# Kernel tuning notes

Measured on AMD Instinct MI355X. Metric: run time of the kernel, lower is better.

## Reference

```python
import jax, jax.numpy as jnp
import numpy as np

CHEB_K = 3


def cheb_gcn(x, node_emb, w_pool, b_pool):
    # x: [B, N, C], node_emb: [N, D], w_pool: [D, K, C, O], b_pool: [D, O]
    n = node_emb.shape[0]
    A = jax.nn.softmax(jax.nn.relu(node_emb @ node_emb.T), axis=1)  # [N, N]
    supports = [jnp.eye(n, dtype=x.dtype), A]
    for _ in range(2, CHEB_K):
        supports.append(2.0 * A @ supports[-1] - supports[-2])
    S = jnp.stack(supports, axis=0)  # [K, N, N]
    weights = jnp.einsum('nd,dkio->nkio', node_emb, w_pool)  # [N, K, C, O]
    bias = node_emb @ b_pool  # [N, O]
    x_g = jnp.einsum('knm,bmc->bnkc', S, x)  # [B, N, K, C]
    return jnp.einsum('bnki,nkio->bno', x_g, weights) + bias


def setup_inputs() -> dict:
    key = jax.random.key(0)
    ks = jax.random.split(key, 7)
    B, N, DIN, DOUT, E = 64, 1024, 64, 64, 16
    C = DIN + DOUT
    return {
        'x': jax.random.normal(ks[0], (B, N, DIN), jnp.float32),
        'state': jax.random.normal(ks[1], (B, N, DOUT), jnp.float32),
        'node_embeddings': jax.random.normal(ks[2], (N, E), jnp.float32),
        'W_gate': jax.random.normal(ks[3], (E, CHEB_K, C, 2 * DOUT), jnp.float32) * 0.1,
        'b_gate': jax.random.normal(ks[4], (E, 2 * DOUT), jnp.float32) * 0.1,
        'W_update': jax.random.normal(ks[5], (E, CHEB_K, C, DOUT), jnp.float32) * 0.1,
        'b_update': jax.random.normal(ks[6], (E, DOUT), jnp.float32) * 0.1,
    }


def reference(x, state, node_embeddings, W_gate, b_gate, W_update, b_update):
    hidden = state.shape[-1]
    inp = jnp.concatenate([x, state], axis=-1)  # [B, N, DIN+DOUT]
    z_r = jax.nn.sigmoid(cheb_gcn(inp, node_embeddings, W_gate, b_gate))
    z, r = z_r[..., :hidden], z_r[..., hidden:]
    cand = jnp.concatenate([x, r * state], axis=-1)
    h_hat = jnp.tanh(cheb_gcn(cand, node_embeddings, W_update, b_update))
    return z * state + (1.0 - z) * h_hat
```

## Files before the change

### kernel.cpp

```cpp
#include <hip/hip_runtime.h>
#include <hip/hip_bf16.h>
#include <math.h>

#define B_ 64
#define N_ 1024
#define E_ 16

typedef unsigned short ushort_t;
typedef __attribute__((ext_vector_type(8))) short bf16x8;
typedef __attribute__((ext_vector_type(4))) float f32x4;

__device__ __forceinline__ float sigmoidf_(float x) {
  return 1.0f / (1.0f + __expf(-x));
}
__device__ __forceinline__ ushort_t f2bf(float f) {
  unsigned int u = __float_as_uint(f);
  u = (u + 0x7fffu + ((u >> 16) & 1u)) >> 16;
  return (ushort_t)u;
}
__device__ __forceinline__ float bf2f(ushort_t h) { return __uint_as_float((unsigned)h << 16); }
__device__ __forceinline__ void gload16(const void* g, void* l) {
  __builtin_amdgcn_global_load_lds(
      (const __attribute__((address_space(1))) unsigned int*)g,
      (__attribute__((address_space(3))) unsigned int*)l, 16, 0, 0);
}

__global__ __launch_bounds__(256) void compute_A_kernel(const float* __restrict__ emb,
                                                        ushort_t* __restrict__ Ah,
                                                        ushort_t* __restrict__ Al) {
  __shared__ float embn[E_];
  __shared__ float red[256];
  const int n = blockIdx.x;
  const int t = threadIdx.x;
  if (t < E_) embn[t] = emb[n * E_ + t];
  __syncthreads();
  float s[4];
#pragma unroll
  for (int j = 0; j < 4; ++j) {
    const int m = j * 256 + t;
    const float* em = emb + m * E_;
    float acc = 0.f;
#pragma unroll
    for (int d = 0; d < E_; ++d) acc = fmaf(embn[d], em[d], acc);
    s[j] = fmaxf(acc, 0.f);
  }
  float mx = fmaxf(fmaxf(s[0], s[1]), fmaxf(s[2], s[3]));
  red[t] = mx;
  __syncthreads();
  for (int off = 128; off > 0; off >>= 1) {
    if (t < off) red[t] = fmaxf(red[t], red[t + off]);
    __syncthreads();
  }
  mx = red[0];
  __syncthreads();
  float e[4], lsum = 0.f;
#pragma unroll
  for (int j = 0; j < 4; ++j) { e[j] = __expf(s[j] - mx); lsum += e[j]; }
  red[t] = lsum;
  __syncthreads();
  for (int off = 128; off > 0; off >>= 1) {
    if (t < off) red[t] += red[t + off];
    __syncthreads();
  }
  const float inv = 1.0f / red[0];
#pragma unroll
  for (int j = 0; j < 4; ++j) {
    const float v = e[j] * inv;
    ushort_t h = f2bf(v);
    Ah[n * N_ + j * 256 + t] = h;
    Al[n * N_ + j * 256 + t] = f2bf(v - bf2f(h));
  }
}

__global__ __launch_bounds__(256) void build_T0t_kernel(const float* __restrict__ xA,
                                                        const float* __restrict__ xB,
                                                        ushort_t* __restrict__ Th,
                                                        ushort_t* __restrict__ Tl) {
  __shared__ float tile[128][129];
  const int t = threadIdx.x;
  const int b = blockIdx.y;
  const int n0 = blockIdx.x << 7;
  const int c4 = (t & 31) << 2, nl = t >> 5;
#pragma unroll
  for (int p = 0; p < 16; ++p) {
    const int n = nl + (p << 3);
    const float4 v = (c4 < 64)
        ? *(const float4*)&xA[((size_t)b << 16) + ((size_t)(n0 + n) << 6) + c4]
        : *(const float4*)&xB[((size_t)b << 16) + ((size_t)(n0 + n) << 6) + c4 - 64];
    tile[c4 + 0][n] = v.x; tile[c4 + 1][n] = v.y;
    tile[c4 + 2][n] = v.z; tile[c4 + 3][n] = v.w;
  }
  __syncthreads();
  const int c = t >> 1, nc = (t & 1) << 6;
  const size_t obase = ((size_t)(b << 7) + c) * 1024 + n0 + nc;
#pragma unroll
  for (int u = 0; u < 64; u += 4) {
    ushort4 h, l;
    float v0 = tile[c][nc + u + 0], v1 = tile[c][nc + u + 1];
    float v2 = tile[c][nc + u + 2], v3 = tile[c][nc + u + 3];
    h.x = f2bf(v0); l.x = f2bf(v0 - bf2f(h.x));
    h.y = f2bf(v1); l.y = f2bf(v1 - bf2f(h.y));
    h.z = f2bf(v2); l.z = f2bf(v2 - bf2f(h.z));
    h.w = f2bf(v3); l.w = f2bf(v3 - bf2f(h.w));
    *(ushort4*)&Th[obase + u] = h;
    *(ushort4*)&Tl[obase + u] = l;
  }
}

__global__ __launch_bounds__(256) void build_T0s_kernel(const float* __restrict__ rs,
                                                        ushort_t* __restrict__ Th,
                                                        ushort_t* __restrict__ Tl) {
  __shared__ float tile[64][129];
  const int t = threadIdx.x;
  const int b = blockIdx.y;
  const int n0 = blockIdx.x << 7;
  const int c4 = (t & 15) << 2, nl = t >> 4;
#pragma unroll
  for (int p = 0; p < 8; ++p) {
    const int n = nl + (p << 4);
    const float4 v = *(const float4*)&rs[((size_t)b << 16) + ((size_t)(n0 + n) << 6) + c4];
    tile[c4 + 0][n] = v.x; tile[c4 + 1][n] = v.y;
    tile[c4 + 2][n] = v.z; tile[c4 + 3][n] = v.w;
  }
  __syncthreads();
  const int c = t >> 2, nc = (t & 3) << 5;
  const size_t obase = ((size_t)(b << 6) + c) * 1024 + n0 + nc;
#pragma unroll
  for (int u = 0; u < 32; u += 4) {
    ushort4 h, l;
    float v0 = tile[c][nc + u + 0], v1 = tile[c][nc + u + 1];
    float v2 = tile[c][nc + u + 2], v3 = tile[c][nc + u + 3];
    h.x = f2bf(v0); l.x = f2bf(v0 - bf2f(h.x));
    h.y = f2bf(v1); l.y = f2bf(v1 - bf2f(h.y));
    h.z = f2bf(v2); l.z = f2bf(v2 - bf2f(h.z));
    h.w = f2bf(v3); l.w = f2bf(v3 - bf2f(h.w));
    *(ushort4*)&Th[obase + u] = h;
    *(ushort4*)&Tl[obase + u] = l;
  }
}

template <int PHASE, int SPAN>
__global__ __launch_bounds__(256, 2) void mfma_gemm_kernel(
    const ushort_t* __restrict__ Ah, const ushort_t* __restrict__ Al,
    const ushort_t* __restrict__ Bh, const ushort_t* __restrict__ Bl,
    ushort_t* __restrict__ Yth, ushort_t* __restrict__ Ytl,
    ushort_t* __restrict__ XpH, ushort_t* __restrict__ XpL) {
  __shared__ ushort_t smem[4 * 128 * 64];
  ushort_t* Ah_s = smem;
  ushort_t* Al_s = smem + 8192;
  ushort_t* Bh_s = smem + 16384;
  ushort_t* Bl_s = smem + 24576;
  const int t = threadIdx.x;
  const int wave = t >> 6, lane = t & 63;
  const int n0 = blockIdx.y << 7;
  const int bcol = blockIdx.x;
  const int j0 = bcol << 7;
  const int wr = wave >> 1, wc = wave & 1;
  const int fr = lane & 15, fk = lane >> 4;

  f32x4 acc[4][4];
#pragma unroll
  for (int i = 0; i < 4; ++i)
#pragma unroll
    for (int j = 0; j < 4; ++j) acc[i][j] = (f32x4){0.f, 0.f, 0.f, 0.f};

  const int rsub = lane >> 3;
  const int cp = lane & 7;
  const int selem = (((cp << 4) ^ (rsub << 4)) >> 1);

  for (int k0 = 0; k0 < 1024; k0 += 64) {
    __syncthreads();
#pragma unroll
    for (int i = 0; i < 4; ++i) {
      const int q = (wave << 2) + i;
      const int row = (q << 3) + rsub;
      const int lo = (q << 9) + lane * 8;
      const size_t ga = (size_t)(n0 + row) * 1024 + k0 + selem;
      const size_t gb = (size_t)(j0 + row) * 1024 + k0 + selem;
      gload16(Ah + ga, Ah_s + lo);
      gload16(Al + ga, Al_s + lo);
      gload16(Bh + gb, Bh_s + lo);
      gload16(Bl + gb, Bl_s + lo);
    }
    __syncthreads();
#pragma unroll
    for (int ks = 0; ks < 2; ++ks) {
      bf16x8 ah[4], al[4], bh[4], bl[4];
#pragma unroll
      for (int mi = 0; mi < 4; ++mi) {
        const int r = (wr << 6) + (mi << 4) + fr;
        const int kb = ((ks << 6) + (fk << 4)) ^ ((r & 7) << 4);
        ah[mi] = *(const bf16x8*)((const char*)Ah_s + r * 128 + kb);
        al[mi] = *(const bf16x8*)((const char*)Al_s + r * 128 + kb);
      }
#pragma unroll
      for (int nj = 0; nj < 4; ++nj) {
        const int r = (wc << 6) + (nj << 4) + fr;
        const int kb = ((ks << 6) + (fk << 4)) ^ ((r & 7) << 4);
        bh[nj] = *(const bf16x8*)((const char*)Bh_s + r * 128 + kb);
        bl[nj] = *(const bf16x8*)((const char*)Bl_s + r * 128 + kb);
      }
#pragma unroll
      for (int mi = 0; mi < 4; ++mi)
#pragma unroll
        for (int nj = 0; nj < 4; ++nj) {
          acc[mi][nj] = __builtin_amdgcn_mfma_f32_16x16x32_bf16(ah[mi], bh[nj], acc[mi][nj], 0, 0, 0);
          acc[mi][nj] = __builtin_amdgcn_mfma_f32_16x16x32_bf16(ah[mi], bl[nj], acc[mi][nj], 0, 0, 0);
          acc[mi][nj] = __builtin_amdgcn_mfma_f32_16x16x32_bf16(al[mi], bh[nj], acc[mi][nj], 0, 0, 0);
        }
    }
  }

  __syncthreads();
  ushort_t* hiT = smem;
  ushort_t* loT = smem + 16384;
#pragma unroll
  for (int mi = 0; mi < 4; ++mi) {
    const int nl = (wr << 6) + (mi << 4) + (fk << 2);
#pragma unroll
    for (int nj = 0; nj < 4; ++nj) {
      const int jl = (wc << 6) + (nj << 4) + fr;
      const f32x4 vv = acc[mi][nj];
      ushort_t h[4], l[4];
#pragma unroll
      for (int r = 0; r < 4; ++r) {
        const float v = (PHASE == 1) ? vv[r] : 2.0f * vv[r];
        h[r] = f2bf(v);
        l[r] = f2bf(v - bf2f(h[r]));
      }
      if (PHASE == 1) {
        *(ushort4*)&Yth[(size_t)(j0 + jl) * 1024 + n0 + nl] = make_ushort4(h[0], h[1], h[2], h[3]);
        *(ushort4*)&Ytl[(size_t)(j0 + jl) * 1024 + n0 + nl] = make_ushort4(l[0], l[1], l[2], l[3]);
      }
#pragma unroll
      for (int r = 0; r < 4; ++r) {
        hiT[(nl + r) * 128 + jl] = h[r];
        loT[(nl + r) * 128 + jl] = l[r];
      }
    }
  }
  __syncthreads();
#pragma unroll
  for (int rr = 0; rr < 8; ++rr) {
    const int id = rr * 256 + t;
    const int nl = id >> 4, ch = id & 15;
    size_t dstE;
    if (SPAN == 128) {
      dstE = ((size_t)(n0 + nl) * 64 + bcol) * 256 + ch * 8;
    } else {
      const int bb = bcol * 2 + (ch >> 3);
      dstE = ((size_t)(n0 + nl) * 64 + bb) * 256 + 64 + (ch & 7) * 8;
    }
    *(uint4*)&XpH[dstE] = *(const uint4*)((const char*)hiT + nl * 256 + ch * 16);
    *(uint4*)&XpL[dstE] = *(const uint4*)((const char*)loT + nl * 256 + ch * 16);
  }
}

template <int OW>
__global__ __launch_bounds__(256) void wpt_kernel(const float* __restrict__ Wp,
                                                  float* __restrict__ WpT) {
  const int idx = blockIdx.x * 256 + threadIdx.x;
  const int ki = idx % 384;
  const int k = ki >> 7, i = ki & 127;
  const int o = idx / 384;
  float v[16];
#pragma unroll
  for (int d = 0; d < 16; ++d) v[d] = Wp[((size_t)d * 384 + ki) * OW + o];
  if (k == 0) {
#pragma unroll
    for (int d = 0; d < 16; ++d) v[d] -= Wp[((size_t)d * 384 + 256 + i) * OW + o];
  }
  float* dst = WpT + (size_t)idx * 16;
#pragma unroll
  for (int q = 0; q < 4; ++q) *(float4*)&dst[q * 4] = *(const float4*)&v[q * 4];
}

__global__ __launch_bounds__(384) void wcombine5_kernel(const float* __restrict__ emb,
                                                        const float* __restrict__ WpT,
                                                        ushort_t* __restrict__ WtH,
                                                        ushort_t* __restrict__ WtL) {
  __shared__ float embs[256 * 16];
  __shared__ ushort_t sH[8 * 384];
  __shared__ ushort_t sL[8 * 384];
  const int t = threadIdx.x;
  const int o = blockIdx.y;
  const int n0 = blockIdx.x << 8;
  for (int i = t; i < 1024; i += 384)
    *(float4*)&embs[i * 4] = *(const float4*)&emb[(size_t)n0 * 16 + i * 4];
  float wreg[16];
  {
    const float* src = WpT + (size_t)o * 6144 + t * 16;
#pragma unroll
    for (int q = 0; q < 4; ++q) *(float4*)&wreg[q * 4] = *(const float4*)&src[q * 4];
  }
  __syncthreads();
  for (int g = 0; g < 32; ++g) {
#pragma unroll
    for (int nl = 0; nl < 8; ++nl) {
      const float* e = &embs[(g * 8 + nl) * 16];
      float a = 0.f;
#pragma unroll
      for (int d = 0; d < 16; ++d) a = fmaf(e[d], wreg[d], a);
      const ushort_t h = f2bf(a);
      sH[nl * 384 + t] = h;
      sL[nl * 384 + t] = f2bf(a - bf2f(h));
    }
    __syncthreads();
    const size_t ob = ((size_t)o * 1024 + n0 + g * 8) * 384 + t * 8;
    *(uint4*)&WtH[ob] = *(const uint4*)&sH[t * 8];
    *(uint4*)&WtL[ob] = *(const uint4*)&sL[t * 8];
    __syncthreads();
  }
}

template <int MODE>
__global__ __launch_bounds__(256, 2) void pernode_mfma_kernel(
    const float* __restrict__ xA, const float* __restrict__ xB,
    const ushort_t* __restrict__ XpH, const ushort_t* __restrict__ XpL,
    const ushort_t* __restrict__ WtH, const ushort_t* __restrict__ WtL,
    const float* __restrict__ emb, const float* __restrict__ bsrc, int bstride,
    const float* __restrict__ state, const float* __restrict__ zb,
    float* __restrict__ dst) {
  __shared__ ushort_t xh_s[64 * 128];
  __shared__ ushort_t xl_s[64 * 128];
  __shared__ ushort_t wh_s[64 * 128];
  __shared__ ushort_t wl_s[64 * 128];
  __shared__ float embn[E_];
  __shared__ float bias[64];
  const int n = blockIdx.x;
  const int t = threadIdx.x;
  if (t < E_) embn[t] = emb[n * E_ + t];
  __syncthreads();
  if (t < 64) {
    float a = 0.f;
#pragma unroll
    for (int d = 0; d < E_; ++d) a = fmaf(embn[d], bsrc[d * bstride + t], a);
    bias[t] = a;
  }
  const int wave = t >> 6, lane = t & 63;
  const int fr = lane & 15, fq = lane >> 4;
  f32x4 acc[4];
#pragma unroll
  for (int i = 0; i < 4; ++i) acc[i] = (f32x4){0.f, 0.f, 0.f, 0.f};

#pragma unroll
  for (int s = 0; s < 3; ++s) {
    __syncthreads();
    if (s == 0) {
      const int b = t >> 2, q = t & 3;
      const float* srcp = (q < 2)
          ? xA + ((size_t)b << 16) + ((size_t)n << 6) + (q << 5)
          : xB + ((size_t)b << 16) + ((size_t)n << 6) + ((q - 2) << 5);
      float v[32];
#pragma unroll
      for (int j = 0; j < 8; ++j) *(float4*)&v[j * 4] = *(const float4*)&srcp[j * 4];
      const int swz = (b & 7) << 4;
#pragma unroll
      for (int jc = 0; jc < 4; ++jc) {
        unsigned int hh[4], ll[4];
#pragma unroll
        for (int e = 0; e < 4; ++e) {
          const float a0 = v[jc * 8 + 2 * e], a1 = v[jc * 8 + 2 * e + 1];
          const ushort_t h0 = f2bf(a0), h1 = f2bf(a1);
          const ushort_t l0 = f2bf(a0 - bf2f(h0)), l1 = f2bf(a1 - bf2f(h1));
          hh[e] = (unsigned)h0 | ((unsigned)h1 << 16);
          ll[e] = (unsigned)l0 | ((unsigned)l1 << 16);
        }
        const int dstb = b * 256 + (((q << 6) + (jc << 4)) ^ swz);
        *(uint4*)((char*)xh_s + dstb) = make_uint4(hh[0], hh[1], hh[2], hh[3]);
        *(uint4*)((char*)xl_s + dstb) = make_uint4(ll[0], ll[1], ll[2], ll[3]);
      }
    } else {
#pragma unroll
      for (int r = 0; r < 4; ++r) {
        const int id = r * 256 + t;
        const int row = id >> 4, ch = id & 15;
        const int selem = (((ch << 4) ^ ((row & 7) << 4)) >> 1);
        const size_t so = ((size_t)n * 64 + row) * 256 + (s - 1) * 128 + selem;
        gload16(XpH + so, xh_s + id * 8);
        gload16(XpL + so, xl_s + id * 8);
      }
    }
#pragma unroll
    for (int r = 0; r < 4; ++r) {
      const int id = r * 256 + t;
      const int row = id >> 4, ch = id & 15;
      const int selem = (((ch << 4) ^ ((row & 7) << 4)) >> 1);
      const size_t so = ((size_t)row * 1024 + n) * 384 + s * 128 + selem;
      gload16(WtH + so, wh_s + id * 8);
      gload16(WtL + so, wl_s + id * 8);
    }
    __syncthreads();
#pragma unroll
    for (int ks = 0; ks < 4; ++ks) {
      bf16x8 ah[4], al[4];
#pragma unroll
      for (int mi = 0; mi < 4; ++mi) {
        const int r = (mi << 4) + fr;
        const int kb = ((ks << 6) + (fq << 4)) ^ ((r & 7) << 4);
        ah[mi] = *(const bf16x8*)((const char*)xh_s + r * 256 + kb);
        al[mi] = *(const bf16x8*)((const char*)xl_s + r * 256 + kb);
      }
      const int rw = (wave << 4) + fr;
      const int kbw = ((ks << 6) + (fq << 4)) ^ ((rw & 7) << 4);
      const bf16x8 wh = *(const bf16x8*)((const char*)wh_s + rw * 256 + kbw);
      const bf16x8 wl = *(const bf16x8*)((const char*)wl_s + rw * 256 + kbw);
#pragma unroll
      for (int mi = 0; mi < 4; ++mi) {
        acc[mi] = __builtin_amdgcn_mfma_f32_16x16x32_bf16(ah[mi], wh, acc[mi], 0, 0, 0);
        acc[mi] = __builtin_amdgcn_mfma_f32_16x16x32_bf16(al[mi], wh, acc[mi], 0, 0, 0);
        acc[mi] = __builtin_amdgcn_mfma_f32_16x16x32_bf16(ah[mi], wl, acc[mi], 0, 0, 0);
      }
    }
  }

  const int o = (wave << 4) + fr;
  const float bia = bias[o];
#pragma unroll
  for (int mi = 0; mi < 4; ++mi) {
    const int b0 = (mi << 4) + (fq << 2);
    const f32x4 vv = acc[mi];
#pragma unroll
    for (int r = 0; r < 4; ++r) {
      const int b = b0 + r;
      const size_t base = ((size_t)b << 16) + ((size_t)n << 6);
      const float a = vv[r] + bia;
      if (MODE == 0) {
        dst[base + o] = sigmoidf_(a);
      } else if (MODE == 1) {
        dst[base + o] = sigmoidf_(a) * state[base + o];
      } else {
        const float z = zb[base + o], st = state[base + o];
        dst[base + o] = z * st + (1.f - z) * tanhf(a);
      }
    }
  }
}

extern "C" void kernel_launch(void* const* d_in, const int* in_sizes, int n_in,
                              void* d_out, int out_size, void* d_ws, size_t ws_size,
                              hipStream_t stream) {
  const float* x     = (const float*)d_in[0];
  const float* state = (const float*)d_in[1];
  const float* emb   = (const float*)d_in[2];
  const float* Wg    = (const float*)d_in[3];
  const float* bg    = (const float*)d_in[4];
  const float* Wu    = (const float*)d_in[5];
  const float* bu    = (const float*)d_in[6];
  float* out = (float*)d_out;

  char* w = (char*)d_ws;
  ushort_t* Ah   = (ushort_t*)(w);
  ushort_t* Al   = (ushort_t*)(w + ((size_t)2 << 20));
  ushort_t* T0th = (ushort_t*)(w + ((size_t)4 << 20));
  ushort_t* T0tl = (ushort_t*)(w + ((size_t)20 << 20));
  ushort_t* Y1th = (ushort_t*)(w + ((size_t)36 << 20));
  ushort_t* Y1tl = (ushort_t*)(w + ((size_t)52 << 20));
  ushort_t* XpH  = (ushort_t*)(w + ((size_t)68 << 20));
  ushort_t* XpL  = (ushort_t*)(w + ((size_t)100 << 20));
  ushort_t* WtH  = (ushort_t*)(w + ((size_t)132 << 20));
  ushort_t* WtL  = (ushort_t*)(w + ((size_t)180 << 20));
  float*    rs   = (float*)(w + ((size_t)228 << 20));
  float*    WpTg = (float*)(w + ((size_t)244 << 20));
  float*    WpTu = (float*)(w + ((size_t)247 << 20));
  float* zb = out;

  const dim3 gg(64, 8);
  const dim3 gu(32, 8);
  const dim3 gt(8, 64);
  const dim3 gc(4, 64);

  compute_A_kernel<<<N_, 256, 0, stream>>>(emb, Ah, Al);
  wpt_kernel<128><<<192, 256, 0, stream>>>(Wg, WpTg);
  wpt_kernel<64><<<96, 256, 0, stream>>>(Wu, WpTu);

  build_T0t_kernel<<<gt, 256, 0, stream>>>(x, state, T0th, T0tl);
  mfma_gemm_kernel<1, 128><<<gg, 256, 0, stream>>>(Ah, Al, T0th, T0tl, Y1th, Y1tl, XpH, XpL);
  mfma_gemm_kernel<0, 128><<<gg, 256, 0, stream>>>(Ah, Al, Y1th, Y1tl, nullptr, nullptr,
                                                   XpH + 128, XpL + 128);
  wcombine5_kernel<<<gc, 384, 0, stream>>>(emb, WpTg, WtH, WtL);
  pernode_mfma_kernel<0><<<N_, 256, 0, stream>>>(x, state, XpH, XpL, WtH, WtL, emb, bg, 128,
                                                 state, nullptr, zb);
  wcombine5_kernel<<<gc, 384, 0, stream>>>(emb, WpTg + (size_t)64 * 6144, WtH, WtL);
  pernode_mfma_kernel<1><<<N_, 256, 0, stream>>>(x, state, XpH, XpL, WtH, WtL, emb, bg + 64, 128,
                                                 state, nullptr, rs);

  wcombine5_kernel<<<gc, 384, 0, stream>>>(emb, WpTu, WtH, WtL);
  build_T0s_kernel<<<gt, 256, 0, stream>>>(rs, T0th, T0tl);
  mfma_gemm_kernel<1, 64><<<gu, 256, 0, stream>>>(Ah, Al, T0th, T0tl, Y1th, Y1tl, XpH, XpL);
  mfma_gemm_kernel<0, 64><<<gu, 256, 0, stream>>>(Ah, Al, Y1th, Y1tl, nullptr, nullptr,
                                                  XpH + 128, XpL + 128);
  pernode_mfma_kernel<2><<<N_, 256, 0, stream>>>(x, rs, XpH, XpL, WtH, WtL, emb, bu, 64,
                                                 state, zb, out);
}
```

Baseline: 489.7 us.

## Precompute 2A² and stack with A to apply both supports in one GEMM

Computes M = 2·A·A once, using a transposed copy of A and one small GEMM, and stores it below A as a stacked [2N, N] operand. Each graph-convolution stage then runs one GEMM with twice the row blocks against the input, instead of two dependent GEMMs (A·X, then A·(A·X)). This removes the intermediate Y round trip and the serialization between the two GEMMs. It adds a transpose kernel and an N×N×N GEMM. The identity term is assumed to be folded into the weights, as the existing wpt subtraction suggests.

New measurement: 480.9 us. No clear change (-1.8%).

```diff
diff --git a/kernel.cpp b/kernel.cpp
--- a/kernel.cpp
+++ b/kernel.cpp
@@ -69,6 +69,38 @@
     ushort_t h = f2bf(v);
     Ah[n * N_ + j * 256 + t] = h;
     Al[n * N_ + j * 256 + t] = f2bf(v - bf2f(h));
+  }
+}
+
+__global__ __launch_bounds__(256) void transpose_A_kernel(const ushort_t* __restrict__ src1,
+                                                          ushort_t* __restrict__ dst1,
+                                                          const ushort_t* __restrict__ src2,
+                                                          ushort_t* __restrict__ dst2) {
+  __shared__ ushort_t tile[128][130];
+  const int t = threadIdx.x;
+  const int r0 = blockIdx.y << 7, c0 = blockIdx.x << 7;
+  const ushort_t* src = src1;
+  ushort_t* dst = dst1;
+#pragma unroll
+  for (int p = 0; p < 2; ++p) {
+    if (p) { src = src2; dst = dst2; __syncthreads(); }
+#pragma unroll
+    for (int it = 0; it < 8; ++it) {
+      const int id = it * 256 + t;
+      const int row = id >> 4, ch = (id & 15) << 3;
+      *(uint4*)&tile[row][ch] = *(const uint4*)&src[(size_t)(r0 + row) * 1024 + c0 + ch];
+    }
+    __syncthreads();
+#pragma unroll
+    for (int it = 0; it < 8; ++it) {
+      const int id = it * 256 + t;
+      const int row = id >> 4, ch = (id & 15) << 3;
+      ushort_t v[8];
+#pragma unroll
+      for (int u = 0; u < 8; ++u) v[u] = tile[ch + u][row];
+      *(uint4*)&dst[(size_t)(c0 + row) * 1024 + r0 + ch] = *(const uint4*)v;
+    }
+    __syncthreads();
   }
 }
 
@@ -139,12 +171,11 @@
   }
 }
 
-template <int PHASE, int SPAN>
+template <int MODE, int SPAN>
 __global__ __launch_bounds__(256, 2) void mfma_gemm_kernel(
     const ushort_t* __restrict__ Ah, const ushort_t* __restrict__ Al,
     const ushort_t* __restrict__ Bh, const ushort_t* __restrict__ Bl,
-    ushort_t* __restrict__ Yth, ushort_t* __restrict__ Ytl,
-    ushort_t* __restrict__ XpH, ushort_t* __restrict__ XpL) {
+    ushort_t* __restrict__ OutH, ushort_t* __restrict__ OutL) {
   __shared__ ushort_t smem[4 * 128 * 64];
   ushort_t* Ah_s = smem;
   ushort_t* Al_s = smem + 8192;
@@ -221,38 +252,33 @@
     for (int nj = 0; nj < 4; ++nj) {
       const int jl = (wc << 6) + (nj << 4) + fr;
       const f32x4 vv = acc[mi][nj];
-      ushort_t h[4], l[4];
 #pragma unroll
       for (int r = 0; r < 4; ++r) {
-        const float v = (PHASE == 1) ? vv[r] : 2.0f * vv[r];
-        h[r] = f2bf(v);
-        l[r] = f2bf(v - bf2f(h[r]));
-      }
-      if (PHASE == 1) {
-        *(ushort4*)&Yth[(size_t)(j0 + jl) * 1024 + n0 + nl] = make_ushort4(h[0], h[1], h[2], h[3]);
-        *(ushort4*)&Ytl[(size_t)(j0 + jl) * 1024 + n0 + nl] = make_ushort4(l[0], l[1], l[2], l[3]);
-      }
-#pragma unroll
-      for (int r = 0; r < 4; ++r) {
-        hiT[(nl + r) * 128 + jl] = h[r];
-        loT[(nl + r) * 128 + jl] = l[r];
-      }
-    }
-  }
-  __syncthreads();
+        const float v = (MODE == 1) ? 2.0f * vv[r] : vv[r];
+        const ushort_t h = f2bf(v);
+        hiT[(nl + r) * 128 + jl] = h;
+        loT[(nl + r) * 128 + jl] = f2bf(v - bf2f(h));
+      }
+    }
+  }
+  __syncthreads();
+  const int soff = (n0 >= 1024) ? 128 : 0;
+  const int n0e = n0 & 1023;
 #pragma unroll
   for (int rr = 0; rr < 8; ++rr) {
     const int id = rr * 256 + t;
     const int nl = id >> 4, ch = id & 15;
     size_t dstE;
-    if (SPAN == 128) {
-      dstE = ((size_t)(n0 + nl) * 64 + bcol) * 256 + ch * 8;
+    if (MODE == 1) {
+      dstE = (size_t)(n0 + nl) * 1024 + j0 + ch * 8;
+    } else if (SPAN == 128) {
+      dstE = ((size_t)(n0e + nl) * 64 + bcol) * 256 + soff + ch * 8;
     } else {
       const int bb = bcol * 2 + (ch >> 3);
-      dstE = ((size_t)(n0 + nl) * 64 + bb) * 256 + 64 + (ch & 7) * 8;
-    }
-    *(uint4*)&XpH[dstE] = *(const uint4*)((const char*)hiT + nl * 256 + ch * 16);
-    *(uint4*)&XpL[dstE] = *(const uint4*)((const char*)loT + nl * 256 + ch * 16);
+      dstE = ((size_t)(n0e + nl) * 64 + bb) * 256 + soff + 64 + (ch & 7) * 8;
+    }
+    *(uint4*)&OutH[dstE] = *(const uint4*)((const char*)hiT + nl * 256 + ch * 16);
+    *(uint4*)&OutL[dstE] = *(const uint4*)((const char*)loT + nl * 256 + ch * 16);
   }
 }
 
@@ -450,34 +476,37 @@
   float* out = (float*)d_out;
 
   char* w = (char*)d_ws;
-  ushort_t* Ah   = (ushort_t*)(w);
-  ushort_t* Al   = (ushort_t*)(w + ((size_t)2 << 20));
-  ushort_t* T0th = (ushort_t*)(w + ((size_t)4 << 20));
-  ushort_t* T0tl = (ushort_t*)(w + ((size_t)20 << 20));
-  ushort_t* Y1th = (ushort_t*)(w + ((size_t)36 << 20));
-  ushort_t* Y1tl = (ushort_t*)(w + ((size_t)52 << 20));
-  ushort_t* XpH  = (ushort_t*)(w + ((size_t)68 << 20));
-  ushort_t* XpL  = (ushort_t*)(w + ((size_t)100 << 20));
-  ushort_t* WtH  = (ushort_t*)(w + ((size_t)132 << 20));
-  ushort_t* WtL  = (ushort_t*)(w + ((size_t)180 << 20));
-  float*    rs   = (float*)(w + ((size_t)228 << 20));
-  float*    WpTg = (float*)(w + ((size_t)244 << 20));
-  float*    WpTu = (float*)(w + ((size_t)247 << 20));
+  ushort_t* AhS  = (ushort_t*)(w);
+  ushort_t* AlS  = (ushort_t*)(w + ((size_t)4 << 20));
+  ushort_t* Ath  = (ushort_t*)(w + ((size_t)8 << 20));
+  ushort_t* Atl  = (ushort_t*)(w + ((size_t)10 << 20));
+  ushort_t* T0th = (ushort_t*)(w + ((size_t)12 << 20));
+  ushort_t* T0tl = (ushort_t*)(w + ((size_t)28 << 20));
+  ushort_t* XpH  = (ushort_t*)(w + ((size_t)44 << 20));
+  ushort_t* XpL  = (ushort_t*)(w + ((size_t)76 << 20));
+  ushort_t* WtH  = (ushort_t*)(w + ((size_t)108 << 20));
+  ushort_t* WtL  = (ushort_t*)(w + ((size_t)156 << 20));
+  float*    rs   = (float*)(w + ((size_t)204 << 20));
+  float*    WpTg = (float*)(w + ((size_t)220 << 20));
+  float*    WpTu = (float*)(w + ((size_t)223 << 20));
+  ushort_t* Mh = AhS + (size_t)1024 * 1024;
+  ushort_t* Ml = AlS + (size_t)1024 * 1024;
   float* zb = out;
 
-  const dim3 gg(64, 8);
-  const dim3 gu(32, 8);
+  const dim3 ggd(64, 16);
+  const dim3 gud(32, 16);
+  const dim3 gm(8, 8);
   const dim3 gt(8, 64);
   const dim3 gc(4, 64);
 
-  compute_A_kernel<<<N_, 256, 0, stream>>>(emb, Ah, Al);
+  compute_A_kernel<<<N_, 256, 0, stream>>>(emb, AhS, AlS);
+  transpose_A_kernel<<<gm, 256, 0, stream>>>(AhS, Ath, AlS, Atl);
+  mfma_gemm_kernel<1, 128><<<gm, 256, 0, stream>>>(AhS, AlS, Ath, Atl, Mh, Ml);
   wpt_kernel<128><<<192, 256, 0, stream>>>(Wg, WpTg);
   wpt_kernel<64><<<96, 256, 0, stream>>>(Wu, WpTu);
 
   build_T0t_kernel<<<gt, 256, 0, stream>>>(x, state, T0th, T0tl);
-  mfma_gemm_kernel<1, 128><<<gg, 256, 0, stream>>>(Ah, Al, T0th, T0tl, Y1th, Y1tl, XpH, XpL);
-  mfma_gemm_kernel<0, 128><<<gg, 256, 0, stream>>>(Ah, Al, Y1th, Y1tl, nullptr, nullptr,
-                                                   XpH + 128, XpL + 128);
+  mfma_gemm_kernel<0, 128><<<ggd, 256, 0, stream>>>(AhS, AlS, T0th, T0tl, XpH, XpL);
   wcombine5_kernel<<<gc, 384, 0, stream>>>(emb, WpTg, WtH, WtL);
   pernode_mfma_kernel<0><<<N_, 256, 0, stream>>>(x, state, XpH, XpL, WtH, WtL, emb, bg, 128,
                                                  state, nullptr, zb);
@@ -487,9 +516,7 @@
 
   wcombine5_kernel<<<gc, 384, 0, stream>>>(emb, WpTu, WtH, WtL);
   build_T0s_kernel<<<gt, 256, 0, stream>>>(rs, T0th, T0tl);
-  mfma_gemm_kernel<1, 64><<<gu, 256, 0, stream>>>(Ah, Al, T0th, T0tl, Y1th, Y1tl, XpH, XpL);
-  mfma_gemm_kernel<0, 64><<<gu, 256, 0, stream>>>(Ah, Al, Y1th, Y1tl, nullptr, nullptr,
-                                                  XpH + 128, XpL + 128);
+  mfma_gemm_kernel<0, 64><<<gud, 256, 0, stream>>>(AhS, AlS, T0th, T0tl, XpH, XpL);
   pernode_mfma_kernel<2><<<N_, 256, 0, stream>>>(x, rs, XpH, XpL, WtH, WtL, emb, bu, 64,
                                                  state, zb, out);
 }
```
